# Kernel optimization log

Hardware: AMD Instinct MI355X
Metric: run time of the kernel (lower is better)

## Reference

```python
import jax, jax.numpy as jnp
import numpy as np

NUM_EXPERTS = 8
D_IN = 128
INTERMEDIATE_SIZE = 16
B, T = 16, 4096


def setup_inputs() -> dict:
    key = jax.random.key(0)
    k1, k2, k3, k4 = jax.random.split(key, 4)
    x = jax.random.normal(k1, (B, T, D_IN), dtype=jnp.float32)
    routing_weights = jax.random.uniform(k2, (B, T, NUM_EXPERTS), dtype=jnp.float32)
    w1 = jax.random.normal(k3, (NUM_EXPERTS, D_IN, INTERMEDIATE_SIZE), dtype=jnp.float32)
    w2 = jax.random.normal(k4, (NUM_EXPERTS, INTERMEDIATE_SIZE, D_IN), dtype=jnp.float32)
    return {"x": x, "routing_weights": routing_weights, "w1": w1, "w2": w2}


def reference(x, routing_weights, w1, w2):
    # x: [B,T,D], w1: [E,D,I] -> y: [B,T,E,I]  (broadcasting replaces torch expand)
    y = jnp.einsum('btc,eci->btei', x, w1)
    y = jax.nn.gelu(y, approximate=False)  # matches torch F.gelu default (exact erf)
    # y: [B,T,E,I], w2: [E,I,D] -> experts_out: [B,T,E,D]
    moe_experts_out = jnp.einsum('btei,eic->btec', y, w2)
    # weighted combine over experts
    moe_agg = jnp.einsum('btec,bte->btc', moe_experts_out, routing_weights)
    return (moe_agg, moe_experts_out)
```

## Files before the change

### kernel.cpp

```cpp
#include <hip/hip_runtime.h>
#include <math.h>

#define NEXP 8
#define DIN 128
#define NTOK (16 * 4096)

#define LPITCH 136
#define LDS_PER_WAVE (16 * LPITCH)
#define SMEM_BYTES (4 * LDS_PER_WAVE * 4)

typedef float f32x4 __attribute__((ext_vector_type(4)));
typedef unsigned int u32;
typedef u32 u32x2 __attribute__((ext_vector_type(2)));
typedef u32 u32x4 __attribute__((ext_vector_type(4)));
typedef short short8 __attribute__((ext_vector_type(8)));

__device__ __forceinline__ u32 pk2(float lo, float hi) {
    return ((__float_as_uint(hi) + 0x8000u) & 0xffff0000u) |
           ((__float_as_uint(lo) + 0x8000u) >> 16);
}

__global__ void pack_weights_kernel(const float* __restrict__ w1,
                                    const float* __restrict__ w2,
                                    u32* __restrict__ P1u,
                                    u32* __restrict__ P2u) {
    int idx = blockIdx.x * 256 + threadIdx.x;
    if (idx < 8192) {
        int c     = idx & 3;
        int entry = idx >> 2;
        int l     = entry & 63;
        int nbkb  = entry >> 6;
        int nb = nbkb >> 2, kb = nbkb & 3;
        int qq = l >> 4, row = l & 15;
        int ch = kb * 32 + qq * 8 + 2 * c;
        const float* s = w1 + nb * 2048 + ch * 16 + row;
        P1u[idx] = pk2(s[0], s[16]);
    } else {
        int j     = idx - 8192;
        int c2    = j & 3;
        int entry = j >> 2;
        int l     = entry & 63;
        int ecp   = entry >> 6;
        int e = ecp >> 2, cp = ecp & 3;
        int s = c2 >> 1, c = c2 & 1;
        int i0 = (l >> 4) * 4 + 2 * c;
        int outc = (2 * cp + s) * 16 + (l & 15);
        const float* src = w2 + e * 2048 + i0 * 128 + outc;
        P2u[j] = pk2(src[0], src[128]);
    }
}

__global__ __launch_bounds__(256, 1) __attribute__((amdgpu_num_vgpr(128)))
void moe_mfma_kernel(
    const float* __restrict__ x,
    const float* __restrict__ rw,
    const unsigned short* __restrict__ P1,
    const u32* __restrict__ P2,
    float* __restrict__ out_agg,
    float* __restrict__ out_exp)
{
    extern __shared__ float lds[];

    const int tid  = threadIdx.x;
    const int wave = tid >> 6;
    const int lane = tid & 63;
    const int q    = lane >> 4;
    const int n16  = lane & 15;
    const int wtok = blockIdx.x * 64 + wave * 16;

    float* Lw = lds + wave * LDS_PER_WAVE;

    short8 b1[4];
    {
        const float* xb = x + (size_t)(wtok + n16) * DIN + q * 8;
#pragma unroll
        for (int kb = 0; kb < 4; ++kb) {
            f32x4 lo = *(const f32x4*)(xb + kb * 32);
            f32x4 hi = *(const f32x4*)(xb + kb * 32 + 4);
            u32x4 u;
            u.x = pk2(lo.x, lo.y); u.y = pk2(lo.z, lo.w);
            u.z = pk2(hi.x, hi.y); u.w = pk2(hi.z, hi.w);
            b1[kb] = __builtin_bit_cast(short8, u);
        }
    }

    const short8* P1f = (const short8*)P1;
    f32x4 c1[8];
#pragma unroll
    for (int nb = 0; nb < 8; ++nb) {
        f32x4 a = {0.f, 0.f, 0.f, 0.f};
#pragma unroll
        for (int kb = 0; kb < 4; ++kb) {
            short8 af = P1f[(nb * 4 + kb) * 64 + lane];
            a = __builtin_amdgcn_mfma_f32_16x16x32_bf16(af, b1[kb], a, 0, 0, 0);
        }
        c1[nb] = a;
    }

    u32x2 pa[8];
#pragma unroll
    for (int e = 0; e < 8; ++e) {
        float g0 = c1[e][0], g1 = c1[e][1], g2 = c1[e][2], g3 = c1[e][3];
        g0 = 0.5f * g0 * (1.f + erff(g0 * 0.70710678118654752f));
        g1 = 0.5f * g1 * (1.f + erff(g1 * 0.70710678118654752f));
        g2 = 0.5f * g2 * (1.f + erff(g2 * 0.70710678118654752f));
        g3 = 0.5f * g3 * (1.f + erff(g3 * 0.70710678118654752f));
        pa[e].x = pk2(g0, g1);
        pa[e].y = pk2(g2, g3);
    }

    const u32x4* P2f = (const u32x4*)P2;
    f32x4 aggs[8];
#pragma unroll
    for (int cb = 0; cb < 8; ++cb) aggs[cb] = (f32x4){0.f, 0.f, 0.f, 0.f};

    const size_t tok = (size_t)(wtok + n16);
    const f32x4 z = {0.f, 0.f, 0.f, 0.f};
    const int rtok = (lane >> 5);
    const int rc   = (lane & 31) * 4;
    const float* rwp = rw + tok * NEXP;

#pragma unroll
    for (int e = 0; e < 8; ++e) {
        u32x4 au = {pa[e].x, pa[e].y, pa[e].x, pa[e].y};
        short8 gfrag = __builtin_bit_cast(short8, au);
        const float rwe = rwp[e];

#pragma unroll
        for (int cp = 0; cp < 4; ++cp) {
            u32x4 W = P2f[(e * 4 + cp) * 64 + lane];
            {
                u32x4 wu = {W.x, W.y, 0u, 0u};
                short8 wf = __builtin_bit_cast(short8, wu);
                f32x4 o = __builtin_amdgcn_mfma_f32_16x16x32_bf16(wf, gfrag, z, 0, 0, 0);
                *(f32x4*)(Lw + n16 * LPITCH + (2 * cp) * 16 + 4 * q) = o;
                aggs[2 * cp] += rwe * o;
            }
            {
                u32x4 wu = {W.z, W.w, 0u, 0u};
                short8 wf = __builtin_bit_cast(short8, wu);
                f32x4 o = __builtin_amdgcn_mfma_f32_16x16x32_bf16(wf, gfrag, z, 0, 0, 0);
                *(f32x4*)(Lw + n16 * LPITCH + (2 * cp + 1) * 16 + 4 * q) = o;
                aggs[2 * cp + 1] += rwe * o;
            }
        }

        float* oe = out_exp + (size_t)wtok * (NEXP * DIN) + e * DIN;
#pragma unroll
        for (int k = 0; k < 8; ++k) {
            const int t2 = 2 * k + rtok;
            f32x4 v = *(const f32x4*)(Lw + t2 * LPITCH + rc);
            *(f32x4*)(oe + (size_t)t2 * (NEXP * DIN) + rc) = v;
        }
    }

#pragma unroll
    for (int cb = 0; cb < 8; ++cb)
        *(f32x4*)(Lw + n16 * LPITCH + cb * 16 + 4 * q) = aggs[cb];

    float* oa = out_agg + (size_t)wtok * DIN;
#pragma unroll
    for (int k = 0; k < 8; ++k) {
        const int t2 = 2 * k + rtok;
        f32x4 v = *(const f32x4*)(Lw + t2 * LPITCH + rc);
        *(f32x4*)(oa + (size_t)t2 * DIN + rc) = v;
    }
}

extern "C" void kernel_launch(void* const* d_in, const int* in_sizes, int n_in,
                              void* d_out, int out_size, void* d_ws, size_t ws_size,
                              hipStream_t stream) {
    const float* x  = (const float*)d_in[0];
    const float* rw = (const float*)d_in[1];
    const float* w1 = (const float*)d_in[2];
    const float* w2 = (const float*)d_in[3];

    float* out_agg = (float*)d_out;
    float* out_exp = out_agg + (size_t)NTOK * DIN;
    u32* P1u = (u32*)d_ws;
    u32* P2u = P1u + 8192;

    pack_weights_kernel<<<dim3(64), dim3(256), 0, stream>>>(w1, w2, P1u, P2u);

    dim3 grid(NTOK / 64);
    dim3 block(256);
    moe_mfma_kernel<<<grid, block, SMEM_BYTES, stream>>>(
        x, rw, (const unsigned short*)P1u, P2u, out_agg, out_exp);
}
```

Before: 78.54 us.

## Fuse per-expert GEMM1+GELU into expert loop and defer output stores

Moves the first MFMA GEMM and the erf GELU inside a non-unrolled per-expert loop, so only one expert's intermediate is live at a time instead of all eight. The global store of expert e's output is deferred to the start of iteration e+1, placed before the next GEMM1, with the last expert flushed after the loop. This is meant to cut register pressure and to overlap the LDS-to-global writes with compute. The per-wave LDS buffer is read for e-1 and then rewritten for e in the same wave without a barrier, which relies on in-order execution within the wave. Unroll 1 also adds loop overhead and limits instruction scheduling across experts.

```diff
diff --git a/kernel.cpp b/kernel.cpp
--- a/kernel.cpp
+++ b/kernel.cpp
@@ -85,44 +85,46 @@
     }
 
     const short8* P1f = (const short8*)P1;
-    f32x4 c1[8];
-#pragma unroll
-    for (int nb = 0; nb < 8; ++nb) {
-        f32x4 a = {0.f, 0.f, 0.f, 0.f};
-#pragma unroll
-        for (int kb = 0; kb < 4; ++kb) {
-            short8 af = P1f[(nb * 4 + kb) * 64 + lane];
-            a = __builtin_amdgcn_mfma_f32_16x16x32_bf16(af, b1[kb], a, 0, 0, 0);
-        }
-        c1[nb] = a;
-    }
+    const u32x4*  P2f = (const u32x4*)P2;
 
-    u32x2 pa[8];
-#pragma unroll
-    for (int e = 0; e < 8; ++e) {
-        float g0 = c1[e][0], g1 = c1[e][1], g2 = c1[e][2], g3 = c1[e][3];
-        g0 = 0.5f * g0 * (1.f + erff(g0 * 0.70710678118654752f));
-        g1 = 0.5f * g1 * (1.f + erff(g1 * 0.70710678118654752f));
-        g2 = 0.5f * g2 * (1.f + erff(g2 * 0.70710678118654752f));
-        g3 = 0.5f * g3 * (1.f + erff(g3 * 0.70710678118654752f));
-        pa[e].x = pk2(g0, g1);
-        pa[e].y = pk2(g2, g3);
-    }
-
-    const u32x4* P2f = (const u32x4*)P2;
     f32x4 aggs[8];
 #pragma unroll
     for (int cb = 0; cb < 8; ++cb) aggs[cb] = (f32x4){0.f, 0.f, 0.f, 0.f};
 
     const size_t tok = (size_t)(wtok + n16);
+    const float* rwp = rw + tok * NEXP;
     const f32x4 z = {0.f, 0.f, 0.f, 0.f};
     const int rtok = (lane >> 5);
     const int rc   = (lane & 31) * 4;
-    const float* rwp = rw + tok * NEXP;
+    float* oexp = out_exp + (size_t)wtok * (NEXP * DIN);
 
+#pragma unroll 1
+    for (int e = 0; e < NEXP; ++e) {
+        if (e > 0) {
+            float* oe = oexp + (e - 1) * DIN;
 #pragma unroll
-    for (int e = 0; e < 8; ++e) {
-        u32x4 au = {pa[e].x, pa[e].y, pa[e].x, pa[e].y};
+            for (int k = 0; k < 8; ++k) {
+                const int t2 = 2 * k + rtok;
+                f32x4 v = *(const f32x4*)(Lw + t2 * LPITCH + rc);
+                *(f32x4*)(oe + (size_t)t2 * (NEXP * DIN) + rc) = v;
+            }
+        }
+
+        f32x4 a = {0.f, 0.f, 0.f, 0.f};
+#pragma unroll
+        for (int kb = 0; kb < 4; ++kb) {
+            short8 af = P1f[(e * 4 + kb) * 64 + lane];
+            a = __builtin_amdgcn_mfma_f32_16x16x32_bf16(af, b1[kb], a, 0, 0, 0);
+        }
+
+        float g0 = a[0], g1 = a[1], g2 = a[2], g3 = a[3];
+        g0 = 0.5f * g0 * (1.f + erff(g0 * 0.70710678118654752f));
+        g1 = 0.5f * g1 * (1.f + erff(g1 * 0.70710678118654752f));
+        g2 = 0.5f * g2 * (1.f + erff(g2 * 0.70710678118654752f));
+        g3 = 0.5f * g3 * (1.f + erff(g3 * 0.70710678118654752f));
+        const u32 pa0 = pk2(g0, g1);
+        const u32 pa1 = pk2(g2, g3);
+        u32x4 au = {pa0, pa1, pa0, pa1};
         short8 gfrag = __builtin_bit_cast(short8, au);
         const float rwe = rwp[e];
 
@@ -144,8 +146,10 @@
                 aggs[2 * cp + 1] += rwe * o;
             }
         }
+    }
 
-        float* oe = out_exp + (size_t)wtok * (NEXP * DIN) + e * DIN;
+    {
+        float* oe = oexp + 7 * DIN;
 #pragma unroll
         for (int k = 0; k < 8; ++k) {
             const int t2 = 2 * k + rtok;
```

Result: slower. 82.72 us (+5.3%).
